# Kernel optimization log

Hardware: AMD Instinct MI355X
Metric: run time of the kernel (lower is better)

Reference implementation:

```python
import jax, jax.numpy as jnp
import numpy as np

N_POINTS = 4_194_304
NUM_BATCHES = 4
GRIPPER_DEPTH = 0.1034


def setup_inputs() -> dict:
    key = jax.random.key(0)
    k1, k2, k3, k4, k5 = jax.random.split(key, 5)
    return {
        "points": jax.random.normal(k1, (N_POINTS, 3), dtype=jnp.float32),
        "z1": jax.random.normal(k2, (N_POINTS, 3), dtype=jnp.float32),
        "z2": jax.random.normal(k3, (N_POINTS, 3), dtype=jnp.float32),
        "s": jax.random.normal(k4, (N_POINTS,), dtype=jnp.float32),
        "w": jax.random.uniform(k5, (N_POINTS,), dtype=jnp.float32),
    }


def _normalize(v):
    return v / jnp.linalg.norm(v, axis=-1, keepdims=True)


def reference(points, z1, z2, s, w):
    # --- build_6d_grasps, fully vectorized over all N contact points ---
    base_dirs = z1 / jnp.linalg.norm(z1, axis=1, keepdims=True)          # [N,3]
    inner = jnp.sum(base_dirs * z2, axis=1, keepdims=True)               # [N,1]
    # NOTE: original code divides the projected vector by ||z2|| (faithful)
    approach_dirs = (z2 - inner * base_dirs) / jnp.linalg.norm(z2, axis=1, keepdims=True)

    x_col = _normalize(base_dirs)          # grasp[:3,0]
    z_col = _normalize(approach_dirs)      # grasp[:3,2]
    y_col = _normalize(jnp.cross(z_col, x_col))  # grasp[:3,1]
    # translation: contact + w/2 * x - gripper_depth * z (uses raw w, pre-ReLU)
    t_col = points + (w[:, None] * 0.5) * x_col - GRIPPER_DEPTH * z_col

    top = jnp.stack([x_col, y_col, z_col, t_col], axis=2)  # [N,3,4]
    bottom = jnp.broadcast_to(
        jnp.array([[0.0, 0.0, 0.0, 1.0]], dtype=points.dtype), (points.shape[0], 1, 4)
    )
    grasps = jnp.concatenate([top, bottom], axis=1)  # [N,4,4]

    # --- forward() tail: reshape to batches, sigmoid(s), relu(w) ---
    P = points.shape[0] // NUM_BATCHES
    points_b = points.reshape(NUM_BATCHES, P, 3)
    grasps_b = grasps.reshape(NUM_BATCHES, P, 4, 4)
    s_b = jax.nn.sigmoid(s).reshape(NUM_BATCHES, P)
    w_b = jax.nn.relu(w).reshape(NUM_BATCHES, P)
    return (points_b, grasps_b, s_b, w_b)
```

## Files before the change

### kernel.cpp

```cpp
#include <hip/hip_runtime.h>


typedef float floatx4 __attribute__((ext_vector_type(4)));

constexpr long N_POINTS    = 4194304;
constexpr long GRASP_BASE4 = N_POINTS * 3 / 4;
constexpr long S_BASE4     = N_POINTS * 19 / 4;
constexpr long W_BASE4     = N_POINTS * 20 / 4;

#define GETF(arr, idx) (arr[(idx) >> 2][(idx) & 3])

__global__ __launch_bounds__(256) void contactnet_kernel(
    const floatx4* __restrict__ pts,
    const floatx4* __restrict__ z1v,
    const floatx4* __restrict__ z2v,
    const floatx4* __restrict__ sv,
    const floatx4* __restrict__ wv,
    floatx4* __restrict__ out)
{
    const long t = blockIdx.x * blockDim.x + threadIdx.x;

    floatx4 p[3], u1[3], u2[3];
#pragma unroll
    for (int k = 0; k < 3; ++k) {
        p[k]  = pts[t * 3 + k];
        u1[k] = z1v[t * 3 + k];
        u2[k] = z2v[t * 3 + k];
    }
    const floatx4 s4 = sv[t];
    const floatx4 w4 = wv[t];

#pragma unroll
    for (int k = 0; k < 3; ++k) out[t * 3 + k] = p[k];

    floatx4 sres, wres;

#pragma unroll
    for (int j = 0; j < 4; ++j) {
        const int e = j * 3;
        const float z1x = GETF(u1, e), z1y = GETF(u1, e + 1), z1z = GETF(u1, e + 2);
        const float z2x = GETF(u2, e), z2y = GETF(u2, e + 1), z2z = GETF(u2, e + 2);
        const float px  = GETF(p,  e), py  = GETF(p,  e + 1), pz  = GETF(p,  e + 2);
        const float wf = w4[j];
        const float sf = s4[j];

        const float rn1 = rsqrtf(z1x * z1x + z1y * z1y + z1z * z1z);
        const float bx = z1x * rn1, by = z1y * rn1, bz = z1z * rn1;

        const float inner = bx * z2x + by * z2y + bz * z2z;
        const float rn2 = rsqrtf(z2x * z2x + z2y * z2y + z2z * z2z);
        const float ax = (z2x - inner * bx) * rn2;
        const float ay = (z2y - inner * by) * rn2;
        const float az = (z2z - inner * bz) * rn2;

        const float rna = rsqrtf(ax * ax + ay * ay + az * az);
        const float zx = ax * rna, zy = ay * rna, zz = az * rna;

        const float cx = zy * bz - zz * by;
        const float cy = zz * bx - zx * bz;
        const float cz = zx * by - zy * bx;
        const float rnc = rsqrtf(cx * cx + cy * cy + cz * cz);
        const float yx = cx * rnc, yy = cy * rnc, yz = cz * rnc;

        const float tx = px + 0.5f * wf * bx - 0.1034f * zx;
        const float ty = py + 0.5f * wf * by - 0.1034f * zy;
        const float tz = pz + 0.5f * wf * bz - 0.1034f * zz;

        floatx4 g0, g1, g2, g3;
        g0[0] = bx; g0[1] = yx; g0[2] = zx; g0[3] = tx;
        g1[0] = by; g1[1] = yy; g1[2] = zy; g1[3] = ty;
        g2[0] = bz; g2[1] = yz; g2[2] = zz; g2[3] = tz;
        g3[0] = 0.f; g3[1] = 0.f; g3[2] = 0.f; g3[3] = 1.f;

        const long gb = GRASP_BASE4 + (t * 4 + j) * 4;
        out[gb + 0] = g0;
        out[gb + 1] = g1;
        out[gb + 2] = g2;
        out[gb + 3] = g3;

        sres[j] = 1.0f / (1.0f + __expf(-sf));
        wres[j] = fmaxf(wf, 0.0f);
    }

    out[S_BASE4 + t] = sres;
    out[W_BASE4 + t] = wres;
}

extern "C" void kernel_launch(void* const* d_in, const int* in_sizes, int n_in,
                              void* d_out, int out_size, void* d_ws, size_t ws_size,
                              hipStream_t stream) {
    const floatx4* pts = (const floatx4*)d_in[0];
    const floatx4* z1  = (const floatx4*)d_in[1];
    const floatx4* z2  = (const floatx4*)d_in[2];
    const floatx4* s   = (const floatx4*)d_in[3];
    const floatx4* w   = (const floatx4*)d_in[4];
    floatx4* out = (floatx4*)d_out;

    const int nthreads = (int)(N_POINTS / 4);
    const int block = 256;
    contactnet_kernel<<<nthreads / block, block, 0, stream>>>(pts, z1, z2, s, w, out);
}
```

Baseline: 551.7 us.

## Stage inputs and grasp outputs through LDS for fully coalesced global access

Each block loads its contiguous chunk of points, z1 and z2 with coalesced vector loads into shared memory. Each thread then processes points strided by 256, so the 4x4 grasp matrices are written through a swizzled LDS buffer and stored as contiguous, coalesced 16-byte chunks. The previous version had each thread write 64 bytes per point at strided addresses. The change adds about 52KB of LDS per block and several __syncthreads, which may reduce occupancy.

```diff
diff --git a/kernel.cpp b/kernel.cpp
--- a/kernel.cpp
+++ b/kernel.cpp
@@ -8,8 +8,6 @@
 constexpr long S_BASE4     = N_POINTS * 19 / 4;
 constexpr long W_BASE4     = N_POINTS * 20 / 4;
 
-#define GETF(arr, idx) (arr[(idx) >> 2][(idx) & 3])
-
 __global__ __launch_bounds__(256) void contactnet_kernel(
     const floatx4* __restrict__ pts,
     const floatx4* __restrict__ z1v,
@@ -18,31 +16,50 @@
     const floatx4* __restrict__ wv,
     floatx4* __restrict__ out)
 {
-    const long t = blockIdx.x * blockDim.x + threadIdx.x;
+    __shared__ float   lds_p[3072];
+    __shared__ float   lds_1[3072];
+    __shared__ float   lds_2[3072];
+    __shared__ floatx4 lds_g[1024];
 
-    floatx4 p[3], u1[3], u2[3];
-#pragma unroll
-    for (int k = 0; k < 3; ++k) {
-        p[k]  = pts[t * 3 + k];
-        u1[k] = z1v[t * 3 + k];
-        u2[k] = z2v[t * 3 + k];
-    }
-    const floatx4 s4 = sv[t];
-    const floatx4 w4 = wv[t];
+    const int  tid = threadIdx.x;
+    const long bid = blockIdx.x;
+    const long inb = bid * 768;
 
 #pragma unroll
-    for (int k = 0; k < 3; ++k) out[t * 3 + k] = p[k];
+    for (int i = 0; i < 3; ++i) {
+        const long idx = inb + i * 256 + tid;
+        const floatx4 vp = pts[idx];
+        out[idx] = vp;
+        *reinterpret_cast<floatx4*>(&lds_p[(i * 256 + tid) * 4]) = vp;
+        *reinterpret_cast<floatx4*>(&lds_1[(i * 256 + tid) * 4]) = z1v[idx];
+        *reinterpret_cast<floatx4*>(&lds_2[(i * 256 + tid) * 4]) = z2v[idx];
+    }
 
+    const long swb = bid * 256 + tid;
+    const floatx4 s4 = sv[swb];
+    const floatx4 w4 = wv[swb];
     floatx4 sres, wres;
+#pragma unroll
+    for (int c = 0; c < 4; ++c) {
+        sres[c] = 1.0f / (1.0f + __expf(-s4[c]));
+        wres[c] = fmaxf(w4[c], 0.0f);
+    }
+    out[S_BASE4 + swb] = sres;
+    out[W_BASE4 + swb] = wres;
+
+    __syncthreads();
+
+    const float* __restrict__ wsc = reinterpret_cast<const float*>(wv);
 
 #pragma unroll
     for (int j = 0; j < 4; ++j) {
-        const int e = j * 3;
-        const float z1x = GETF(u1, e), z1y = GETF(u1, e + 1), z1z = GETF(u1, e + 2);
-        const float z2x = GETF(u2, e), z2y = GETF(u2, e + 1), z2z = GETF(u2, e + 2);
-        const float px  = GETF(p,  e), py  = GETF(p,  e + 1), pz  = GETF(p,  e + 2);
-        const float wf = w4[j];
-        const float sf = s4[j];
+        const int q  = j * 256 + tid;
+        const int b3 = q * 3;
+
+        const float px  = lds_p[b3], py  = lds_p[b3 + 1], pz  = lds_p[b3 + 2];
+        const float z1x = lds_1[b3], z1y = lds_1[b3 + 1], z1z = lds_1[b3 + 2];
+        const float z2x = lds_2[b3], z2y = lds_2[b3 + 1], z2z = lds_2[b3 + 2];
+        const float wf  = wsc[bid * 1024 + q];
 
         const float rn1 = rsqrtf(z1x * z1x + z1y * z1y + z1z * z1z);
         const float bx = z1x * rn1, by = z1y * rn1, bz = z1z * rn1;
@@ -67,23 +84,30 @@
         const float tz = pz + 0.5f * wf * bz - 0.1034f * zz;
 
         floatx4 g0, g1, g2, g3;
-        g0[0] = bx; g0[1] = yx; g0[2] = zx; g0[3] = tx;
-        g1[0] = by; g1[1] = yy; g1[2] = zy; g1[3] = ty;
-        g2[0] = bz; g2[1] = yz; g2[2] = zz; g2[3] = tz;
+        g0[0] = bx;  g0[1] = yx;  g0[2] = zx;  g0[3] = tx;
+        g1[0] = by;  g1[1] = yy;  g1[2] = zy;  g1[3] = ty;
+        g2[0] = bz;  g2[1] = yz;  g2[2] = zz;  g2[3] = tz;
         g3[0] = 0.f; g3[1] = 0.f; g3[2] = 0.f; g3[3] = 1.f;
 
-        const long gb = GRASP_BASE4 + (t * 4 + j) * 4;
-        out[gb + 0] = g0;
-        out[gb + 1] = g1;
-        out[gb + 2] = g2;
-        out[gb + 3] = g3;
+        const int sw = (tid >> 1) & 3;
+        lds_g[tid * 4 + (0 ^ sw)] = g0;
+        lds_g[tid * 4 + (1 ^ sw)] = g1;
+        lds_g[tid * 4 + (2 ^ sw)] = g2;
+        lds_g[tid * 4 + (3 ^ sw)] = g3;
 
-        sres[j] = 1.0f / (1.0f + __expf(-sf));
-        wres[j] = fmaxf(wf, 0.0f);
+        __syncthreads();
+
+        const long gb = GRASP_BASE4 + bid * 4096 + (long)j * 1024;
+#pragma unroll
+        for (int k = 0; k < 4; ++k) {
+            const int r  = k * 256 + tid;
+            const int tr = r >> 2;
+            const int kr = r & 3;
+            out[gb + r] = lds_g[tr * 4 + (kr ^ ((tr >> 1) & 3))];
+        }
+
+        __syncthreads();
     }
-
-    out[S_BASE4 + t] = sres;
-    out[W_BASE4 + t] = wres;
 }
 
 extern "C" void kernel_launch(void* const* d_in, const int* in_sizes, int n_in,
@@ -96,7 +120,6 @@
     const floatx4* w   = (const floatx4*)d_in[4];
     floatx4* out = (floatx4*)d_out;
 
-    const int nthreads = (int)(N_POINTS / 4);
-    const int block = 256;
-    contactnet_kernel<<<nthreads / block, block, 0, stream>>>(pts, z1, z2, s, w, out);
+    const int nblocks = (int)(N_POINTS / 1024);
+    contactnet_kernel<<<nblocks, 256, 0, stream>>>(pts, z1, z2, s, w, out);
 }
```

Measured after the change: 480.5 us. -12.9%, faster.
